# Kernel tuning notes

Measured on AMD Instinct MI355X. Metric: run time of the kernel, lower is better.

The kernel has to match this reference:

```python
import jax, jax.numpy as jnp
import numpy as np

EPS = 1e-8  # torch.cosine_similarity norm clamp

def setup_inputs() -> dict:
    key = jax.random.key(0)
    k1, k2, k3, k4 = jax.random.split(key, 4)
    B, S, D, C = 64, 512, 768, 512
    V = jax.random.normal(k1, (B, S, D), dtype=jnp.float32)
    label_embeddings = jax.random.normal(k2, (C, D), dtype=jnp.float32)
    fc_w = jax.random.normal(k3, (C, D), dtype=jnp.float32) * 0.02
    fc_b = jax.random.normal(k4, (C,), dtype=jnp.float32) * 0.02
    return {"V": V, "label_embeddings": label_embeddings, "fc_w": fc_w, "fc_b": fc_b}

def reference(V, label_embeddings, fc_w, fc_b):
    # Normalized embeddings (cosine similarity = dot of unit vectors, norms clamped at EPS)
    Vn = V / jnp.maximum(jnp.linalg.norm(V, axis=-1, keepdims=True), EPS)
    Ln = label_embeddings / jnp.maximum(
        jnp.linalg.norm(label_embeddings, axis=-1, keepdims=True), EPS)
    # [B, S, C] cosine similarities, then max over classes -> per-token weight m [B, S]
    sims = jnp.einsum('bsd,cd->bsc', Vn, Ln)
    m = jnp.max(sims, axis=-1)
    # Softmax over sequence dim -> attention beta [B, S]
    beta = jax.nn.softmax(m, axis=-1)
    # Weighted sum of token embeddings: z = V^T beta  -> [B, D]
    z = jnp.einsum('bsd,bs->bd', V, beta)
    # Final classifier
    out = z @ fc_w.T + fc_b
    return (out, z)
```

## Files before the change

### kernel.cpp

```cpp
#include <hip/hip_runtime.h>
#include <cstdint>
#include <cstddef>

#define BB 64
#define SS 512
#define DD 768
#define CC 512

typedef __attribute__((ext_vector_type(8))) short short8;
typedef __attribute__((ext_vector_type(4))) float f32x4;

#define GLOBAL_AS __attribute__((address_space(1)))
#define LDS_AS __attribute__((address_space(3)))

static __device__ __forceinline__ unsigned short f2bf(float f) {
  union { float f; unsigned u; } v; v.f = f;
  unsigned u = v.u;
  u += 0x7FFFu + ((u >> 16) & 1u);
  return (unsigned short)(u >> 16);
}

static __device__ __forceinline__ void async_copy16(const void* g, void* l) {
  __builtin_amdgcn_global_load_lds((const GLOBAL_AS void*)g, (LDS_AS void*)l,
                                   16, 0, 0);
}

__global__ __launch_bounds__(256) void k_label_norm(const float* __restrict__ L,
                                                    unsigned short* __restrict__ Lnb) {
  const int c = blockIdx.x;
  const int tid = threadIdx.x;
  const float* row = L + (size_t)c * DD;
  float v[3];
  float s = 0.f;
#pragma unroll
  for (int k = 0; k < 3; k++) { v[k] = row[tid + 256 * k]; s += v[k] * v[k]; }
#pragma unroll
  for (int o = 32; o > 0; o >>= 1) s += __shfl_xor(s, o, 64);
  __shared__ float wsum[4];
  if ((tid & 63) == 0) wsum[tid >> 6] = s;
  __syncthreads();
  const float tot = wsum[0] + wsum[1] + wsum[2] + wsum[3];
  const float inv = 1.f / fmaxf(sqrtf(tot), 1e-8f);
  unsigned short* ochunk = Lnb + (size_t)(c >> 4) * (16 * DD);
  const int mr = c & 15;
#pragma unroll
  for (int k = 0; k < 3; k++) {
    const int d = tid + 256 * k;
    const int kc = d >> 5;
    const int q = (d >> 3) & 3;
    const int j = d & 7;
    ochunk[kc * 512 + q * 128 + mr * 8 + j] = f2bf(v[k] * inv);
  }
}

__global__ __launch_bounds__(256) void k_sims_max(const float* __restrict__ V,
                                                  const unsigned short* __restrict__ Lnb,
                                                  float* __restrict__ m_out) {
  const int tid = threadIdx.x;
  const int wave = tid >> 6;
  const int lane = tid & 63;
  const int q = lane >> 4;
  const int mr = lane & 15;
  const int64_t tokBase = (int64_t)blockIdx.x * 64 + wave * 16;

  __shared__ unsigned short Bs[2][16 * DD];
  __shared__ float nrmS[4][16];

  {
    const char* src = (const char*)Lnb;
    char* dst = (char*)&Bs[0][0];
#pragma unroll
    for (int i = wave; i < 24; i += 4)
      async_copy16(src + i * 1024 + lane * 16, dst + i * 1024);
  }

  const float* arow = V + (tokBase + mr) * DD + q * 8;
  short8 afrag[24];
  float nrm2 = 0.f;
#pragma unroll
  for (int kc = 0; kc < 24; kc++) {
    const float4* p = (const float4*)(arow + kc * 32);
    const float4 x = p[0];
    const float4 y = p[1];
    short8 a;
    a[0] = (short)f2bf(x.x); a[1] = (short)f2bf(x.y);
    a[2] = (short)f2bf(x.z); a[3] = (short)f2bf(x.w);
    a[4] = (short)f2bf(y.x); a[5] = (short)f2bf(y.y);
    a[6] = (short)f2bf(y.z); a[7] = (short)f2bf(y.w);
    afrag[kc] = a;
    nrm2 += x.x * x.x + x.y * x.y + x.z * x.z + x.w * x.w;
    nrm2 += y.x * y.x + y.y * y.y + y.z * y.z + y.w * y.w;
  }
  nrm2 += __shfl_xor(nrm2, 16, 64);
  nrm2 += __shfl_xor(nrm2, 32, 64);
  if (q == 0) nrmS[wave][mr] = nrm2;

  __syncthreads();

  const int laneByte = lane * 16;
  f32x4 vmax = {-3e38f, -3e38f, -3e38f, -3e38f};
  for (int cc = 0; cc < 32; cc++) {
    const int p = cc & 1;
    if (cc + 1 < 32) {
      const char* src = (const char*)(Lnb + (size_t)(cc + 1) * 16 * DD);
      char* dst = (char*)&Bs[p ^ 1][0];
#pragma unroll
      for (int i = wave; i < 24; i += 4)
        async_copy16(src + i * 1024 + lane * 16, dst + i * 1024);
    }
    f32x4 acc = {0.f, 0.f, 0.f, 0.f};
    const char* bbase = (const char*)&Bs[p][0] + laneByte;
#pragma unroll
    for (int kc = 0; kc < 24; kc++) {
      const short8 b = *(const short8*)(bbase + kc * 1024);
      acc = __builtin_amdgcn_mfma_f32_16x16x32_bf16(afrag[kc], b, acc, 0, 0, 0);
    }
    vmax[0] = fmaxf(vmax[0], acc[0]);
    vmax[1] = fmaxf(vmax[1], acc[1]);
    vmax[2] = fmaxf(vmax[2], acc[2]);
    vmax[3] = fmaxf(vmax[3], acc[3]);
    __syncthreads();
  }
#pragma unroll
  for (int o = 1; o < 16; o <<= 1) {
#pragma unroll
    for (int r = 0; r < 4; r++) vmax[r] = fmaxf(vmax[r], __shfl_xor(vmax[r], o, 64));
  }
  if (mr == 0) {
#pragma unroll
    for (int r = 0; r < 4; r++) {
      const float nr = nrmS[wave][q * 4 + r];
      m_out[tokBase + q * 4 + r] = vmax[r] / fmaxf(sqrtf(nr), 1e-8f);
    }
  }
}

__global__ __launch_bounds__(256) void k_softmax(const float* __restrict__ m,
                                                 float* __restrict__ beta) {
  const int b = blockIdx.x;
  const int tid = threadIdx.x;
  const float* mb = m + (size_t)b * SS;
  const float v0 = mb[tid];
  const float v1 = mb[tid + 256];
  float mx = fmaxf(v0, v1);
#pragma unroll
  for (int o = 32; o > 0; o >>= 1) mx = fmaxf(mx, __shfl_xor(mx, o, 64));
  __shared__ float wred[4];
  if ((tid & 63) == 0) wred[tid >> 6] = mx;
  __syncthreads();
  mx = fmaxf(fmaxf(wred[0], wred[1]), fmaxf(wred[2], wred[3]));
  const float e0 = __expf(v0 - mx);
  const float e1 = __expf(v1 - mx);
  float s = e0 + e1;
#pragma unroll
  for (int o = 32; o > 0; o >>= 1) s += __shfl_xor(s, o, 64);
  __syncthreads();
  if ((tid & 63) == 0) wred[tid >> 6] = s;
  __syncthreads();
  s = wred[0] + wred[1] + wred[2] + wred[3];
  const float inv = 1.f / s;
  float* bb = beta + (size_t)b * SS;
  bb[tid] = e0 * inv;
  bb[tid + 256] = e1 * inv;
}

__global__ __launch_bounds__(192) void k_zpart(const float* __restrict__ V,
                                               const float* __restrict__ beta,
                                               float* __restrict__ zpart,
                                               int spc, int nsc) {
  const int blk = blockIdx.x;
  const int b = blk / nsc;
  const int sc = blk % nsc;
  const int tid = threadIdx.x;
  const float* vb = V + ((size_t)b * SS + (size_t)sc * spc) * DD + tid * 4;
  const float* bb = beta + (size_t)b * SS + (size_t)sc * spc;
  float4 acc = {0.f, 0.f, 0.f, 0.f};
#pragma unroll 4
  for (int s = 0; s < spc; s++) {
    const float w = bb[s];
    const float4 x = *(const float4*)(vb + (size_t)s * DD);
    acc.x += w * x.x; acc.y += w * x.y; acc.z += w * x.z; acc.w += w * x.w;
  }
  *(float4*)(zpart + (size_t)blk * DD + tid * 4) = acc;
}

__global__ __launch_bounds__(256) void k_final(const float* __restrict__ zpart,
                                               const float* __restrict__ fc_w,
                                               const float* __restrict__ fc_b,
                                               float* __restrict__ out,
                                               float* __restrict__ zout,
                                               int nsc) {
  const int b = blockIdx.x >> 1;
  const int half = blockIdx.x & 1;
  const int tid = threadIdx.x;
  __shared__ float zs[DD];
  for (int i = tid; i < DD; i += 256) {
    float s = 0.f;
    for (int sc = 0; sc < nsc; sc++) s += zpart[((size_t)b * nsc + sc) * DD + i];
    zs[i] = s;
    if (half == 0) zout[(size_t)b * DD + i] = s;
  }
  __syncthreads();
  const int c = half * 256 + tid;
  const float4* w = (const float4*)(fc_w + (size_t)c * DD);
  float acc = 0.f;
  for (int d4 = 0; d4 < DD / 4; d4++) {
    const float4 ww = w[d4];
    acc += ww.x * zs[d4 * 4] + ww.y * zs[d4 * 4 + 1] +
           ww.z * zs[d4 * 4 + 2] + ww.w * zs[d4 * 4 + 3];
  }
  out[(size_t)b * CC + c] = acc + fc_b[c];
}

extern "C" void kernel_launch(void* const* d_in, const int* in_sizes, int n_in,
                              void* d_out, int out_size, void* d_ws, size_t ws_size,
                              hipStream_t stream) {
  const float* V  = (const float*)d_in[0];
  const float* L  = (const float*)d_in[1];
  const float* fw = (const float*)d_in[2];
  const float* fb = (const float*)d_in[3];
  float* out = (float*)d_out;

  char* ws = (char*)d_ws;
  unsigned short* Lnb = (unsigned short*)ws;
  float* m     = (float*)(ws + 786432);
  float* beta  = (float*)(ws + 917504);
  float* zpart = (float*)(ws + 1048576);

  const int nsc = (ws_size >= (size_t)1048576 + (size_t)16 * BB * DD * 4) ? 16 : 8;
  const int spc = SS / nsc;

  k_label_norm<<<CC, 256, 0, stream>>>(L, Lnb);
  k_sims_max<<<512, 256, 0, stream>>>(V, Lnb, m);
  k_softmax<<<BB, 256, 0, stream>>>(m, beta);
  k_zpart<<<BB * nsc, 192, 0, stream>>>(V, beta, zpart, spc, nsc);
  k_final<<<2 * BB, 256, 0, stream>>>(zpart, fw, fb, out, out + BB * CC, nsc);
}
```

Measured before the change: 240.9 us.

## Triple-buffer label tiles in sims kernel with vmcnt-gated barriers

Changes the label-embedding staging in the cosine-similarity/max kernel from double to triple buffering. Each chunk is now prefetched two steps ahead. Each step waits only until the previous chunk's async copies have landed, using `s_waitcnt vmcnt`, a raw barrier and scheduling fences, instead of a full `__syncthreads` per chunk. The goal is to hide global-to-LDS latency behind the MFMA work. In exchange, LDS per block grows from two to three 24 KB buffers, which may reduce how many blocks fit on each compute unit.

```diff
diff --git a/kernel.cpp b/kernel.cpp
--- a/kernel.cpp
+++ b/kernel.cpp
@@ -63,16 +63,21 @@
   const int mr = lane & 15;
   const int64_t tokBase = (int64_t)blockIdx.x * 64 + wave * 16;
 
-  __shared__ unsigned short Bs[2][16 * DD];
+  __shared__ unsigned short Bs[3][16 * DD];
   __shared__ float nrmS[4][16];
 
-  {
-    const char* src = (const char*)Lnb;
-    char* dst = (char*)&Bs[0][0];
+  const int laneByte = lane * 16;
+
+  auto stage = [&](const unsigned short* src, int bufidx) {
+    const char* s = (const char*)src;
+    char* dst = (char*)&Bs[bufidx][0];
 #pragma unroll
     for (int i = wave; i < 24; i += 4)
-      async_copy16(src + i * 1024 + lane * 16, dst + i * 1024);
-  }
+      async_copy16(s + i * 1024 + laneByte, dst + i * 1024);
+  };
+
+  stage(Lnb, 0);
+  stage(Lnb + 16 * DD, 1);
 
   const float* arow = V + (tokBase + mr) * DD + q * 8;
   short8 afrag[24];
@@ -97,19 +102,11 @@
 
   __syncthreads();
 
-  const int laneByte = lane * 16;
   f32x4 vmax = {-3e38f, -3e38f, -3e38f, -3e38f};
-  for (int cc = 0; cc < 32; cc++) {
-    const int p = cc & 1;
-    if (cc + 1 < 32) {
-      const char* src = (const char*)(Lnb + (size_t)(cc + 1) * 16 * DD);
-      char* dst = (char*)&Bs[p ^ 1][0];
-#pragma unroll
-      for (int i = wave; i < 24; i += 4)
-        async_copy16(src + i * 1024 + lane * 16, dst + i * 1024);
-    }
+
+  auto compute = [&](int bufidx) {
+    const char* bbase = (const char*)&Bs[bufidx][0] + laneByte;
     f32x4 acc = {0.f, 0.f, 0.f, 0.f};
-    const char* bbase = (const char*)&Bs[p][0] + laneByte;
 #pragma unroll
     for (int kc = 0; kc < 24; kc++) {
       const short8 b = *(const short8*)(bbase + kc * 1024);
@@ -119,8 +116,34 @@
     vmax[1] = fmaxf(vmax[1], acc[1]);
     vmax[2] = fmaxf(vmax[2], acc[2]);
     vmax[3] = fmaxf(vmax[3], acc[3]);
-    __syncthreads();
-  }
+  };
+
+#define PHASE_BAR(n)                                   \
+  asm volatile("s_waitcnt vmcnt(" #n ")" ::: "memory"); \
+  __builtin_amdgcn_s_barrier();                         \
+  __builtin_amdgcn_sched_barrier(0);
+
+  const unsigned short* srcp = Lnb + (size_t)2 * 16 * DD;
+#pragma unroll 1
+  for (int ccb = 0; ccb < 30; ccb += 3) {
+    stage(srcp, 2); srcp += 16 * DD;
+    __builtin_amdgcn_sched_barrier(0);
+    compute(0);
+    PHASE_BAR(6)
+    stage(srcp, 0); srcp += 16 * DD;
+    __builtin_amdgcn_sched_barrier(0);
+    compute(1);
+    PHASE_BAR(6)
+    stage(srcp, 1); srcp += 16 * DD;
+    __builtin_amdgcn_sched_barrier(0);
+    compute(2);
+    PHASE_BAR(6)
+  }
+  compute(0);
+  PHASE_BAR(0)
+  compute(1);
+#undef PHASE_BAR
+
 #pragma unroll
   for (int o = 1; o < 16; o <<= 1) {
 #pragma unroll
```

After: 251.8 us. 4.5% more time.

## Split class dimension across two blocks in sims-max and merge in softmax

Applied to the files above, without the earlier changes.

The sims-max kernel now launches twice as many blocks, each covering half of the 512 label classes for a 64-token tile. Each half writes its partial max, and the first half also writes the token's squared norm. The softmax kernel combines the two partial maxima and applies the norm division. This raises block count and parallelism across the GPU's compute units. The cost is that every token's V row is loaded and converted to bf16 twice, and there are extra workspace writes and reads.

```diff
diff --git a/kernel.cpp b/kernel.cpp
--- a/kernel.cpp
+++ b/kernel.cpp
@@ -55,19 +55,24 @@
 
 __global__ __launch_bounds__(256) void k_sims_max(const float* __restrict__ V,
                                                   const unsigned short* __restrict__ Lnb,
-                                                  float* __restrict__ m_out) {
+                                                  float* __restrict__ mpart,
+                                                  float* __restrict__ nrm_out) {
   const int tid = threadIdx.x;
   const int wave = tid >> 6;
   const int lane = tid & 63;
   const int q = lane >> 4;
   const int mr = lane & 15;
-  const int64_t tokBase = (int64_t)blockIdx.x * 64 + wave * 16;
+  const int tile = blockIdx.x >> 1;
+  const int half = blockIdx.x & 1;
+  const int64_t tokBase = (int64_t)tile * 64 + wave * 16;
 
   __shared__ unsigned short Bs[2][16 * DD];
   __shared__ float nrmS[4][16];
 
+  const unsigned short* chunks = Lnb + (size_t)(half * 16) * 16 * DD;
+
   {
-    const char* src = (const char*)Lnb;
+    const char* src = (const char*)chunks;
     char* dst = (char*)&Bs[0][0];
 #pragma unroll
     for (int i = wave; i < 24; i += 4)
@@ -99,10 +104,10 @@
 
   const int laneByte = lane * 16;
   f32x4 vmax = {-3e38f, -3e38f, -3e38f, -3e38f};
-  for (int cc = 0; cc < 32; cc++) {
+  for (int cc = 0; cc < 16; cc++) {
     const int p = cc & 1;
-    if (cc + 1 < 32) {
-      const char* src = (const char*)(Lnb + (size_t)(cc + 1) * 16 * DD);
+    if (cc + 1 < 16) {
+      const char* src = (const char*)(chunks + (size_t)(cc + 1) * 16 * DD);
       char* dst = (char*)&Bs[p ^ 1][0];
 #pragma unroll
       for (int i = wave; i < 24; i += 4)
@@ -129,19 +134,23 @@
   if (mr == 0) {
 #pragma unroll
     for (int r = 0; r < 4; r++) {
-      const float nr = nrmS[wave][q * 4 + r];
-      m_out[tokBase + q * 4 + r] = vmax[r] / fmaxf(sqrtf(nr), 1e-8f);
+      mpart[(size_t)half * (BB * SS) + tokBase + q * 4 + r] = vmax[r];
+      if (half == 0) nrm_out[tokBase + q * 4 + r] = nrmS[wave][q * 4 + r];
     }
   }
 }
 
-__global__ __launch_bounds__(256) void k_softmax(const float* __restrict__ m,
+__global__ __launch_bounds__(256) void k_softmax(const float* __restrict__ mpart,
+                                                 const float* __restrict__ nrm,
                                                  float* __restrict__ beta) {
   const int b = blockIdx.x;
   const int tid = threadIdx.x;
-  const float* mb = m + (size_t)b * SS;
-  const float v0 = mb[tid];
-  const float v1 = mb[tid + 256];
+  const size_t i0 = (size_t)b * SS + tid;
+  const size_t i1 = i0 + 256;
+  const float v0 = fmaxf(mpart[i0], mpart[i0 + BB * SS]) /
+                   fmaxf(sqrtf(nrm[i0]), 1e-8f);
+  const float v1 = fmaxf(mpart[i1], mpart[i1 + BB * SS]) /
+                   fmaxf(sqrtf(nrm[i1]), 1e-8f);
   float mx = fmaxf(v0, v1);
 #pragma unroll
   for (int o = 32; o > 0; o >>= 1) mx = fmaxf(mx, __shfl_xor(mx, o, 64));
@@ -223,16 +232,17 @@
 
   char* ws = (char*)d_ws;
   unsigned short* Lnb = (unsigned short*)ws;
-  float* m     = (float*)(ws + 786432);
-  float* beta  = (float*)(ws + 917504);
-  float* zpart = (float*)(ws + 1048576);
-
-  const int nsc = (ws_size >= (size_t)1048576 + (size_t)16 * BB * DD * 4) ? 16 : 8;
+  float* mpart = (float*)(ws + 786432);
+  float* nrm   = (float*)(ws + 1048576);
+  float* beta  = (float*)(ws + 1179648);
+  float* zpart = (float*)(ws + 1310720);
+
+  const int nsc = (ws_size >= (size_t)1310720 + (size_t)16 * BB * DD * 4) ? 16 : 8;
   const int spc = SS / nsc;
 
   k_label_norm<<<CC, 256, 0, stream>>>(L, Lnb);
-  k_sims_max<<<512, 256, 0, stream>>>(V, Lnb, m);
-  k_softmax<<<BB, 256, 0, stream>>>(m, beta);
+  k_sims_max<<<1024, 256, 0, stream>>>(V, Lnb, mpart, nrm);
+  k_softmax<<<BB, 256, 0, stream>>>(mpart, nrm, beta);
   k_zpart<<<BB * nsc, 192, 0, stream>>>(V, beta, zpart, spc, nsc);
   k_final<<<2 * BB, 256, 0, stream>>>(zpart, fw, fb, out, out + BB * CC, nsc);
 }
```

Result: slower. 260.7 us (+8.2%).
